# Performance work log

Measured on AMD Instinct MI355X. Metric: run time of the kernel, lower is better.

Reference implementation:

```python
import jax, jax.numpy as jnp
import numpy as np

RADIUS = 0.1
NSAMPLE = 32
B, N, NPOINT, C = 2, 16384, 4096, 64


def setup_inputs() -> dict:
    key = jax.random.key(0)
    k1, k2, k3 = jax.random.split(key, 3)
    xyz = jax.random.uniform(k1, (B, N, 3), dtype=jnp.float32)
    new_xyz = jax.random.uniform(k2, (B, NPOINT, 3), dtype=jnp.float32)
    features = jax.random.normal(k3, (B, C, N), dtype=jnp.float32)
    return {"xyz": xyz, "new_xyz": new_xyz, "features": features}


def ball_query(radius, nsample, xyz, new_xyz):
    # xyz: (B, N, 3), new_xyz: (B, npoint, 3) -> idx: (B, npoint, nsample) int32
    # Semantics of the CUDA ball_query: take the first `nsample` points (in
    # original order) whose squared distance < radius^2; pad remaining slots
    # with the first in-ball index (0 if the ball is empty).
    d2 = jnp.sum((new_xyz[:, :, None, :] - xyz[:, None, :, :]) ** 2, axis=-1)  # (B, npoint, N)
    mask = d2 < radius * radius
    # stable argsort puts in-ball indices first, preserving original order
    order = jnp.argsort(jnp.where(mask, 0, 1), axis=-1)  # (B, npoint, N)
    cnt = jnp.sum(mask, axis=-1, keepdims=True)  # (B, npoint, 1)
    first = jnp.where(cnt > 0, order[..., :1], 0)  # (B, npoint, 1)
    slots = jnp.arange(nsample)
    idx = jnp.where(slots < cnt, order[..., :nsample], first)
    return idx.astype(jnp.int32)


def group(features, idx):
    # features: (B, C, N), idx: (B, npoint, nsample) -> (B, C, npoint, nsample)
    return jax.vmap(lambda f, i: f[:, i])(features, idx)


def reference(xyz, new_xyz, features):
    idx = ball_query(RADIUS, NSAMPLE, xyz, new_xyz)  # (B, npoint, nsample)
    xyz_t = jnp.transpose(xyz, (0, 2, 1))  # (B, 3, N)
    grouped_xyz = group(xyz_t, idx)  # (B, 3, npoint, nsample)
    grouped_xyz = grouped_xyz - jnp.transpose(new_xyz, (0, 2, 1))[..., None]
    grouped_features = group(features, idx)  # (B, C, npoint, nsample)
    new_features = jnp.concatenate([grouped_xyz, grouped_features], axis=1)
    return new_features  # (B, 3 + C, npoint, nsample)
```

## Files before the change

### kernel.cpp

```cpp
#include <hip/hip_runtime.h>

#define B 2
#define N 16384
#define NPOINT 4096
#define C 64
#define NSAMPLE 32

#define NCELL 1000
#define CELLW_STRIDE 1024
#define OFF_STRIDE 1056
#define CAP 192

#define HIST_BLOCKS ((B * (N + NPOINT) + 255) / 256)
#define TRANS_BLOCKS (B * (N / 64))

__device__ __forceinline__ float r2_thresh() { return (float)(0.1 * 0.1); }

__device__ __forceinline__ int clamp09(int v) { return v < 0 ? 0 : (v > 9 ? 9 : v); }

__device__ __forceinline__ int cell_of(float x, float y, float z) {
    const int ix = clamp09((int)floorf(x * 10.0f));
    const int iy = clamp09((int)floorf(y * 10.0f));
    const int iz = clamp09((int)floorf(z * 10.0f));
    return (ix * 10 + iy) * 10 + iz;
}

__global__ void __launch_bounds__(256) hist_transpose_kernel(
    const float* __restrict__ xyz, const float* __restrict__ new_xyz,
    int* __restrict__ cellwork, int* __restrict__ qwork,
    const float* __restrict__ feat, float* __restrict__ ft) {
    __shared__ float tile[64 * 65];
    const int t = threadIdx.x;

    if (blockIdx.x >= HIST_BLOCKS) {
        const int tb = blockIdx.x - HIST_BLOCKS;
        const int b = tb / (N / 64);
        const int n0 = (tb % (N / 64)) * 64;
        const int l = t & 63;
        const int w = t >> 6;
#pragma unroll
        for (int it = 0; it < 16; ++it) {
            const int c = it * 4 + w;
            tile[c * 65 + l] = feat[((size_t)b * C + c) * N + n0 + l];
        }
        __syncthreads();
#pragma unroll
        for (int it = 0; it < 16; ++it) {
            const int nn = it * 4 + w;
            ft[((size_t)b * N + n0 + nn) * C + l] = tile[l * 65 + nn];
        }
        return;
    }

    const int i = blockIdx.x * blockDim.x + t;
    if (i < B * N) {
        const int b = i / N;
        const float x = xyz[(size_t)i * 3 + 0];
        const float y = xyz[(size_t)i * 3 + 1];
        const float z = xyz[(size_t)i * 3 + 2];
        atomicAdd(&cellwork[b * CELLW_STRIDE + cell_of(x, y, z)], 1);
    } else if (i < B * (N + NPOINT)) {
        const int qi = i - B * N;
        const int b = qi / NPOINT;
        const float x = new_xyz[(size_t)qi * 3 + 0];
        const float y = new_xyz[(size_t)qi * 3 + 1];
        const float z = new_xyz[(size_t)qi * 3 + 2];
        atomicAdd(&qwork[b * CELLW_STRIDE + cell_of(x, y, z)], 1);
    }
}

__global__ void __launch_bounds__(1024) grid_scan_kernel(
    int* __restrict__ cellwork, int* __restrict__ qwork, int* __restrict__ off) {
    __shared__ int wsum[16];
    const int blk = blockIdx.x;
    const int t = threadIdx.x;
    const int lane = t & 63;
    const int w = t >> 6;
    int* __restrict__ arr = (blk < B) ? (cellwork + blk * CELLW_STRIDE)
                                      : (qwork + (blk - B) * CELLW_STRIDE);
    const int v = (t < NCELL) ? arr[t] : 0;

    int s = v;
#pragma unroll
    for (int d = 1; d < 64; d <<= 1) {
        const int u = __shfl_up(s, d, 64);
        if (lane >= d) s += u;
    }
    if (lane == 63) wsum[w] = s;
    __syncthreads();
    if (w == 0) {
        int p = (lane < 16) ? wsum[lane] : 0;
#pragma unroll
        for (int d = 1; d < 16; d <<= 1) {
            const int u = __shfl_up(p, d, 64);
            if (lane >= d) p += u;
        }
        if (lane < 16) wsum[lane] = p;
    }
    __syncthreads();
    const int prefix = (w > 0) ? wsum[w - 1] : 0;
    const int excl = s + prefix - v;
    if (blk < B && t <= NCELL) off[blk * OFF_STRIDE + t] = excl;
    if (t < NCELL) arr[t] = excl;
}

__global__ void __launch_bounds__(256) grid_scatter_kernel(
    const float* __restrict__ xyz, const float* __restrict__ new_xyz,
    int* __restrict__ cellwork, int* __restrict__ qwork,
    float4* __restrict__ binned, int* __restrict__ qperm) {
    const int i = blockIdx.x * blockDim.x + threadIdx.x;
    if (i < B * N) {
        const int b = i / N;
        const int p = i - b * N;
        const float x = xyz[(size_t)i * 3 + 0];
        const float y = xyz[(size_t)i * 3 + 1];
        const float z = xyz[(size_t)i * 3 + 2];
        const int c = cell_of(x, y, z);
        const int pos = atomicAdd(&cellwork[b * CELLW_STRIDE + c], 1);
        float4 v;
        v.x = x; v.y = y; v.z = z; v.w = __int_as_float(p);
        binned[(size_t)b * N + pos] = v;
    } else if (i < B * (N + NPOINT)) {
        const int qi = i - B * N;
        const int b = qi / NPOINT;
        const int j = qi - b * NPOINT;
        const float x = new_xyz[(size_t)qi * 3 + 0];
        const float y = new_xyz[(size_t)qi * 3 + 1];
        const float z = new_xyz[(size_t)qi * 3 + 2];
        const int c = cell_of(x, y, z);
        const int pos = atomicAdd(&qwork[b * CELLW_STRIDE + c], 1);
        qperm[b * NPOINT + pos] = j;
    }
}

__device__ void linear_ball_fallback(const float* __restrict__ xb,
                                     float cx, float cy, float cz,
                                     int lane, unsigned long long lanemask_lt,
                                     int* out) {
    const float r2 = r2_thresh();
    int cnt = 0, first_idx = 0;
    for (int base = 0; base < N; base += 64) {
        const int i = base + lane;
        const float x = xb[i * 3 + 0];
        const float y = xb[i * 3 + 1];
        const float z = xb[i * 3 + 2];
        float d2;
        {
#pragma clang fp contract(off)
            float dx = x - cx;
            float dy = y - cy;
            float dz = z - cz;
            d2 = dx * dx + dy * dy + dz * dz;
        }
        const bool in = d2 < r2;
        const unsigned long long m = __ballot(in);
        if (in) {
            const int pos = cnt + __popcll(m & lanemask_lt);
            if (pos < NSAMPLE) out[pos] = i;
        }
        if (cnt == 0 && m != 0ull) first_idx = base + __builtin_ctzll(m);
        cnt += __popcll(m);
        if (cnt >= NSAMPLE) break;
    }
    if (cnt < NSAMPLE) {
        if (cnt == 0) first_idx = 0;
        for (int pos = cnt + lane; pos < NSAMPLE; pos += 64) out[pos] = first_idx;
    }
}

__device__ __forceinline__ void rank_select(const int* cand, int K, int lane,
                                            int* out) {
    const int e0 = (lane < K) ? cand[lane] : 0x7FFFFFFF;
    const int e1 = (64 + lane < K) ? cand[64 + lane] : 0x7FFFFFFF;
    const int e2 = (128 + lane < K) ? cand[128 + lane] : 0x7FFFFFFF;
    int r0 = 0, r1 = 0, r2i = 0;
    if (K <= 64) {
        for (int k = 0; k < K; ++k) { const int v = cand[k]; r0 += (v < e0); }
    } else if (K <= 128) {
        for (int k = 0; k < K; ++k) { const int v = cand[k]; r0 += (v < e0); r1 += (v < e1); }
    } else {
        for (int k = 0; k < K; ++k) {
            const int v = cand[k];
            r0 += (v < e0); r1 += (v < e1); r2i += (v < e2);
        }
    }
    if (lane < K && r0 < NSAMPLE) out[r0] = e0;
    if (64 + lane < K && r1 < NSAMPLE) out[r1] = e1;
    if (128 + lane < K && r2i < NSAMPLE) out[r2i] = e2;

    if (K < NSAMPLE) {
        int mn = min(e0, min(e1, e2));
#pragma unroll
        for (int d = 32; d; d >>= 1) mn = min(mn, __shfl_xor(mn, d));
        const int fill = (K > 0) ? mn : 0;
        for (int pos = K + lane; pos < NSAMPLE; pos += 64) out[pos] = fill;
    }
}

__device__ __forceinline__ int scan_window(
    const float4* __restrict__ bb, const int* __restrict__ ob,
    int lox, int hix, int loy, int hiy, int loz, int hiz,
    float cx, float cy, float cz, int lane,
    unsigned long long lanemask_lt, int* cand)
{
    const float r2 = r2_thresh();
    int K = 0;
    for (int ix = lox; ix <= hix; ++ix) {
        for (int iy = loy; iy <= hiy; ++iy) {
            const int rowc = (ix * 10 + iy) * 10;
            const int s0 = ob[rowc + loz];
            const int s1 = ob[rowc + hiz + 1];
            for (int cur = s0; cur < s1; cur += 64) {
                const int i = cur + lane;
                const bool valid = (i < s1);
                float4 pv;
                if (valid) pv = bb[i];
                else { pv.x = 1e9f; pv.y = 1e9f; pv.z = 1e9f; pv.w = 0.0f; }
                float d2;
                {
#pragma clang fp contract(off)
                    float dx = pv.x - cx, dy = pv.y - cy, dz = pv.z - cz;
                    d2 = dx * dx + dy * dy + dz * dz;
                }
                const bool in = valid && (d2 < r2);
                const unsigned long long m = __ballot(in);
                if (in) {
                    const int pos = K + __popcll(m & lanemask_lt);
                    if (pos < CAP) cand[pos] = __float_as_int(pv.w);
                }
                K += __popcll(m);
            }
        }
    }
    return K;
}

__global__ void __launch_bounds__(256) fused_kernel(
    const float4* __restrict__ binned,
    const int* __restrict__ off,
    const float* __restrict__ new_xyz,
    const float* __restrict__ xyz,
    const float* __restrict__ ft,
    const int* __restrict__ qperm,
    float* __restrict__ out)
{
    __shared__ int cand_s[4][CAP];
    __shared__ int sidx[4 * NSAMPLE];
    __shared__ int sj[4];
    __shared__ float sf[64 * 65];

    const int t = threadIdx.x;
    const int lane = t & 63;
    const int w = t >> 6;

    const int nwg = B * NPOINT / 4;
    const int g = blockIdx.x;
    const int swz = (g & 7) * (nwg / 8) + (g >> 3);
    const int b = swz / (NPOINT / 4);
    const int p4 = swz % (NPOINT / 4);

    const int j = qperm[b * NPOINT + p4 * 4 + w];
    if (lane == 0) sj[w] = j;

    const float cx = new_xyz[((size_t)b * NPOINT + j) * 3 + 0];
    const float cy = new_xyz[((size_t)b * NPOINT + j) * 3 + 1];
    const float cz = new_xyz[((size_t)b * NPOINT + j) * 3 + 2];

    int* cand = cand_s[w];
    int* sout = sidx + w * NSAMPLE;
    const float4* __restrict__ bb = binned + (size_t)b * N;
    const int* __restrict__ ob = off + b * OFF_STRIDE;

    const unsigned long long lanemask_lt = (lane == 63) ? 0x7FFFFFFFFFFFFFFFull
                                                        : ((1ull << lane) - 1ull);

    const int lox = max(0, (int)floorf((cx - 0.1001f) * 10.0f));
    const int hix = min(9, (int)floorf((cx + 0.1001f) * 10.0f));
    const int loy = max(0, (int)floorf((cy - 0.1001f) * 10.0f));
    const int hiy = min(9, (int)floorf((cy + 0.1001f) * 10.0f));
    const int loz = max(0, (int)floorf((cz - 0.1001f) * 10.0f));
    const int hiz = min(9, (int)floorf((cz + 0.1001f) * 10.0f));

    const int K = scan_window(bb, ob, lox, hix, loy, hiy, loz, hiz,
                              cx, cy, cz, lane, lanemask_lt, cand);

    if (K > CAP) {
        linear_ball_fallback(xyz + (size_t)b * N * 3, cx, cy, cz, lane, lanemask_lt, sout);
    } else {
        rank_select(cand, K, lane, sout);
    }
    __syncthreads();

    const size_t plane = (size_t)NPOINT * NSAMPLE;
    const size_t bbase = (size_t)b * (3 + C) * plane;

    if (t < 128) {
        const int id = sidx[t];
        const int jq = sj[t >> 5];
        const int s = t & 31;
        const size_t cb = ((size_t)b * NPOINT + jq) * 3;
        const size_t pb = ((size_t)b * N + id) * 3;
        const size_t obx = bbase + (size_t)jq * NSAMPLE + s;
        {
#pragma clang fp contract(off)
            out[obx + 0 * plane] = xyz[pb + 0] - new_xyz[cb + 0];
            out[obx + 1 * plane] = xyz[pb + 1] - new_xyz[cb + 1];
            out[obx + 2 * plane] = xyz[pb + 2] - new_xyz[cb + 2];
        }
    }

#pragma unroll
    for (int h = 0; h < 2; ++h) {
        const int* sidxL = sidx + h * 64;
        {
            const int lane16 = t & 15;
            const int pg = t >> 4;
#pragma unroll
            for (int it = 0; it < 4; ++it) {
                const int pp = it * 16 + pg;
                const int id = sidxL[pp];
                const float4 v = *(const float4*)(ft + ((size_t)b * N + id) * C + lane16 * 4);
                float* dst = sf + pp * 65 + lane16 * 4;
                dst[0] = v.x; dst[1] = v.y; dst[2] = v.z; dst[3] = v.w;
            }
        }
        __syncthreads();
        const int q = sj[2 * h + (lane >> 5)];
        const size_t rowbase = bbase + (size_t)q * NSAMPLE + (lane & 31);
#pragma unroll
        for (int it = 0; it < 16; ++it) {
            const int c = it * 4 + w;
            out[rowbase + (size_t)(3 + c) * plane] = sf[lane * 65 + c];
        }
        __syncthreads();
    }
}

__global__ void __launch_bounds__(256) ball_query_kernel(
    const float* __restrict__ xyz, const float* __restrict__ new_xyz,
    int* __restrict__ idx_out)
{
    const int wave = (blockIdx.x * blockDim.x + threadIdx.x) >> 6;
    const int lane = threadIdx.x & 63;
    if (wave >= B * NPOINT) return;
    const int b = wave / NPOINT;
    const float cx = new_xyz[(size_t)wave * 3 + 0];
    const float cy = new_xyz[(size_t)wave * 3 + 1];
    const float cz = new_xyz[(size_t)wave * 3 + 2];
    const unsigned long long lanemask_lt = (lane == 63) ? 0x7FFFFFFFFFFFFFFFull
                                                        : ((1ull << lane) - 1ull);
    linear_ball_fallback(xyz + (size_t)b * N * 3, cx, cy, cz, lane, lanemask_lt,
                         idx_out + (size_t)wave * NSAMPLE);
}

__global__ void __launch_bounds__(256) group_kernel(
    const float* __restrict__ xyz, const float* __restrict__ new_xyz,
    const float* __restrict__ feat, const int* __restrict__ idx_arr,
    float* __restrict__ out) {
    const int t = threadIdx.x;
    const int s = t & 31;
    const int jl = t >> 5;
    const int j = blockIdx.x * 8 + jl;
    const int b = blockIdx.y;

    const int id = idx_arr[((size_t)b * NPOINT + j) * NSAMPLE + s];

    const float px = xyz[((size_t)b * N + id) * 3 + 0] - new_xyz[((size_t)b * NPOINT + j) * 3 + 0];
    const float py = xyz[((size_t)b * N + id) * 3 + 1] - new_xyz[((size_t)b * NPOINT + j) * 3 + 1];
    const float pz = xyz[((size_t)b * N + id) * 3 + 2] - new_xyz[((size_t)b * NPOINT + j) * 3 + 2];

    const size_t plane = (size_t)NPOINT * NSAMPLE;
    const size_t obase = (size_t)b * (3 + C) * plane + (size_t)j * NSAMPLE + s;

    out[obase + 0 * plane] = px;
    out[obase + 1 * plane] = py;
    out[obase + 2 * plane] = pz;

    const float* __restrict__ fb = feat + (size_t)b * C * N;
#pragma unroll 8
    for (int c = 0; c < C; ++c) {
        out[obase + (size_t)(3 + c) * plane] = fb[(size_t)c * N + id];
    }
}

extern "C" void kernel_launch(void* const* d_in, const int* in_sizes, int n_in,
                              void* d_out, int out_size, void* d_ws, size_t ws_size,
                              hipStream_t stream) {
    const float* xyz     = (const float*)d_in[0];
    const float* new_xyz = (const float*)d_in[1];
    const float* feat    = (const float*)d_in[2];
    float* out = (float*)d_out;

    const size_t idx_bytes    = (size_t)B * NPOINT * NSAMPLE * sizeof(int);
    const size_t ft_bytes     = (size_t)B * N * C * sizeof(float);
    const size_t binned_bytes = (size_t)B * N * sizeof(float4);
    const size_t off_bytes    = (size_t)B * OFF_STRIDE * sizeof(int);
    const size_t cellw_bytes  = (size_t)B * CELLW_STRIDE * sizeof(int);
    const size_t qwork_bytes  = (size_t)B * CELLW_STRIDE * sizeof(int);
    const size_t qperm_bytes  = (size_t)B * NPOINT * sizeof(int);

    char* ws = (char*)d_ws;
    size_t o = 0;
    int*    idx_ws   = (int*)(ws + o);    o += idx_bytes;
    float*  ft       = (float*)(ws + o);  o += ft_bytes;
    float4* binned   = (float4*)(ws + o); o += binned_bytes;
    int*    off      = (int*)(ws + o);    o += off_bytes;
    int*    cellwork = (int*)(ws + o);    o += cellw_bytes;
    int*    qwork    = (int*)(ws + o);    o += qwork_bytes;
    int*    qperm    = (int*)(ws + o);    o += qperm_bytes;

    const bool use_grid = (ws_size >= o);

    if (use_grid) {
        hipMemsetAsync(cellwork, 0, cellw_bytes + qwork_bytes, stream);
        hist_transpose_kernel<<<HIST_BLOCKS + TRANS_BLOCKS, 256, 0, stream>>>(
            xyz, new_xyz, cellwork, qwork, feat, ft);
        grid_scan_kernel<<<2 * B, 1024, 0, stream>>>(cellwork, qwork, off);
        grid_scatter_kernel<<<(B * (N + NPOINT) + 255) / 256, 256, 0, stream>>>(
            xyz, new_xyz, cellwork, qwork, binned, qperm);
        fused_kernel<<<B * NPOINT / 4, 256, 0, stream>>>(
            binned, off, new_xyz, xyz, ft, qperm, out);
    } else {
        ball_query_kernel<<<(B * NPOINT) / 4, 256, 0, stream>>>(xyz, new_xyz, idx_ws);
        dim3 grid2(NPOINT / 8, B);
        group_kernel<<<grid2, 256, 0, stream>>>(xyz, new_xyz, feat, idx_ws, out);
    }
}
```

Measured before the change: 46.86 us.

## Fuse grid scan and scatter into one kernel with shared-memory cursors

Merges the prefix-scan and scatter kernels into one launch per batch and array. Scatter cursors now live in LDS atomics instead of global atomics, which removes a kernel launch and global atomic traffic. The cost is that the scatter runs on only 4 blocks of 1024 threads, which limits parallelism for 32K points. The change also vectorizes the rank_select comparisons with int4 LDS reads (adding sentinel padding to the candidate buffer), prefetches the next segment bounds in scan_window, and makes the window bounds wave-uniform with readfirstlane.

```diff
diff --git a/kernel.cpp b/kernel.cpp
--- a/kernel.cpp
+++ b/kernel.cpp
@@ -69,15 +69,20 @@
     }
 }
 
-__global__ void __launch_bounds__(1024) grid_scan_kernel(
-    int* __restrict__ cellwork, int* __restrict__ qwork, int* __restrict__ off) {
+__global__ void __launch_bounds__(1024) scan_scatter_kernel(
+    const float* __restrict__ xyz, const float* __restrict__ new_xyz,
+    const int* __restrict__ cellwork, const int* __restrict__ qwork,
+    int* __restrict__ off, float4* __restrict__ binned, int* __restrict__ qperm) {
     __shared__ int wsum[16];
+    __shared__ int cur[1024];
     const int blk = blockIdx.x;
     const int t = threadIdx.x;
     const int lane = t & 63;
     const int w = t >> 6;
-    int* __restrict__ arr = (blk < B) ? (cellwork + blk * CELLW_STRIDE)
-                                      : (qwork + (blk - B) * CELLW_STRIDE);
+    const bool is_pts = (blk < B);
+    const int b = is_pts ? blk : blk - B;
+    const int* __restrict__ arr = is_pts ? (cellwork + b * CELLW_STRIDE)
+                                         : (qwork + b * CELLW_STRIDE);
     const int v = (t < NCELL) ? arr[t] : 0;
 
     int s = v;
@@ -100,36 +105,28 @@
     __syncthreads();
     const int prefix = (w > 0) ? wsum[w - 1] : 0;
     const int excl = s + prefix - v;
-    if (blk < B && t <= NCELL) off[blk * OFF_STRIDE + t] = excl;
-    if (t < NCELL) arr[t] = excl;
-}
-
-__global__ void __launch_bounds__(256) grid_scatter_kernel(
-    const float* __restrict__ xyz, const float* __restrict__ new_xyz,
-    int* __restrict__ cellwork, int* __restrict__ qwork,
-    float4* __restrict__ binned, int* __restrict__ qperm) {
-    const int i = blockIdx.x * blockDim.x + threadIdx.x;
-    if (i < B * N) {
-        const int b = i / N;
-        const int p = i - b * N;
-        const float x = xyz[(size_t)i * 3 + 0];
-        const float y = xyz[(size_t)i * 3 + 1];
-        const float z = xyz[(size_t)i * 3 + 2];
-        const int c = cell_of(x, y, z);
-        const int pos = atomicAdd(&cellwork[b * CELLW_STRIDE + c], 1);
-        float4 v;
-        v.x = x; v.y = y; v.z = z; v.w = __int_as_float(p);
-        binned[(size_t)b * N + pos] = v;
-    } else if (i < B * (N + NPOINT)) {
-        const int qi = i - B * N;
-        const int b = qi / NPOINT;
-        const int j = qi - b * NPOINT;
-        const float x = new_xyz[(size_t)qi * 3 + 0];
-        const float y = new_xyz[(size_t)qi * 3 + 1];
-        const float z = new_xyz[(size_t)qi * 3 + 2];
-        const int c = cell_of(x, y, z);
-        const int pos = atomicAdd(&qwork[b * CELLW_STRIDE + c], 1);
-        qperm[b * NPOINT + pos] = j;
+    if (is_pts && t <= NCELL) off[b * OFF_STRIDE + t] = excl;
+    cur[t] = excl;
+    __syncthreads();
+
+    if (is_pts) {
+        for (int i = t; i < N; i += 1024) {
+            const float x = xyz[((size_t)b * N + i) * 3 + 0];
+            const float y = xyz[((size_t)b * N + i) * 3 + 1];
+            const float z = xyz[((size_t)b * N + i) * 3 + 2];
+            const int pos = atomicAdd(&cur[cell_of(x, y, z)], 1);
+            float4 pv;
+            pv.x = x; pv.y = y; pv.z = z; pv.w = __int_as_float(i);
+            binned[(size_t)b * N + pos] = pv;
+        }
+    } else {
+        for (int i = t; i < NPOINT; i += 1024) {
+            const float x = new_xyz[((size_t)b * NPOINT + i) * 3 + 0];
+            const float y = new_xyz[((size_t)b * NPOINT + i) * 3 + 1];
+            const float z = new_xyz[((size_t)b * NPOINT + i) * 3 + 2];
+            const int pos = atomicAdd(&cur[cell_of(x, y, z)], 1);
+            qperm[b * NPOINT + pos] = i;
+        }
     }
 }
 
@@ -168,20 +165,30 @@
     }
 }
 
-__device__ __forceinline__ void rank_select(const int* cand, int K, int lane,
+__device__ __forceinline__ void rank_select(int* cand, int K, int lane,
                                             int* out) {
+    if (lane < 4) cand[K + lane] = 0x7FFFFFFF;
     const int e0 = (lane < K) ? cand[lane] : 0x7FFFFFFF;
     const int e1 = (64 + lane < K) ? cand[64 + lane] : 0x7FFFFFFF;
     const int e2 = (128 + lane < K) ? cand[128 + lane] : 0x7FFFFFFF;
     int r0 = 0, r1 = 0, r2i = 0;
     if (K <= 64) {
-        for (int k = 0; k < K; ++k) { const int v = cand[k]; r0 += (v < e0); }
+        for (int k = 0; k < K; k += 4) {
+            const int4 v = *(const int4*)(cand + k);
+            r0 += (v.x < e0) + (v.y < e0) + (v.z < e0) + (v.w < e0);
+        }
     } else if (K <= 128) {
-        for (int k = 0; k < K; ++k) { const int v = cand[k]; r0 += (v < e0); r1 += (v < e1); }
+        for (int k = 0; k < K; k += 4) {
+            const int4 v = *(const int4*)(cand + k);
+            r0 += (v.x < e0) + (v.y < e0) + (v.z < e0) + (v.w < e0);
+            r1 += (v.x < e1) + (v.y < e1) + (v.z < e1) + (v.w < e1);
+        }
     } else {
-        for (int k = 0; k < K; ++k) {
-            const int v = cand[k];
-            r0 += (v < e0); r1 += (v < e1); r2i += (v < e2);
+        for (int k = 0; k < K; k += 4) {
+            const int4 v = *(const int4*)(cand + k);
+            r0 += (v.x < e0) + (v.y < e0) + (v.z < e0) + (v.w < e0);
+            r1 += (v.x < e1) + (v.y < e1) + (v.z < e1) + (v.w < e1);
+            r2i += (v.x < e2) + (v.y < e2) + (v.z < e2) + (v.w < e2);
         }
     }
     if (lane < K && r0 < NSAMPLE) out[r0] = e0;
@@ -204,33 +211,44 @@
     unsigned long long lanemask_lt, int* cand)
 {
     const float r2 = r2_thresh();
+    const int ny = hiy - loy + 1;
+    const int nseg = (hix - lox + 1) * ny;
     int K = 0;
-    for (int ix = lox; ix <= hix; ++ix) {
-        for (int iy = loy; iy <= hiy; ++iy) {
-            const int rowc = (ix * 10 + iy) * 10;
-            const int s0 = ob[rowc + loz];
-            const int s1 = ob[rowc + hiz + 1];
-            for (int cur = s0; cur < s1; cur += 64) {
-                const int i = cur + lane;
-                const bool valid = (i < s1);
-                float4 pv;
-                if (valid) pv = bb[i];
-                else { pv.x = 1e9f; pv.y = 1e9f; pv.z = 1e9f; pv.w = 0.0f; }
-                float d2;
-                {
+
+    int nix = lox, niy = loy;
+    int a0 = ob[(nix * 10 + niy) * 10 + loz];
+    int b0 = ob[(nix * 10 + niy) * 10 + hiz + 1];
+
+    for (int s = 0; s < nseg; ++s) {
+        int a1 = 0, b1 = 0;
+        if (s + 1 < nseg) {
+            ++niy;
+            if (niy > hiy) { niy = loy; ++nix; }
+            const int rowc = (nix * 10 + niy) * 10;
+            a1 = ob[rowc + loz];
+            b1 = ob[rowc + hiz + 1];
+        }
+        for (int cur = a0; cur < b0; cur += 64) {
+            const int i = cur + lane;
+            const bool valid = (i < b0);
+            float4 pv;
+            if (valid) pv = bb[i];
+            else { pv.x = 1e9f; pv.y = 1e9f; pv.z = 1e9f; pv.w = 0.0f; }
+            float d2;
+            {
 #pragma clang fp contract(off)
-                    float dx = pv.x - cx, dy = pv.y - cy, dz = pv.z - cz;
-                    d2 = dx * dx + dy * dy + dz * dz;
-                }
-                const bool in = valid && (d2 < r2);
-                const unsigned long long m = __ballot(in);
-                if (in) {
-                    const int pos = K + __popcll(m & lanemask_lt);
-                    if (pos < CAP) cand[pos] = __float_as_int(pv.w);
-                }
-                K += __popcll(m);
+                float dx = pv.x - cx, dy = pv.y - cy, dz = pv.z - cz;
+                d2 = dx * dx + dy * dy + dz * dz;
             }
-        }
+            const bool in = valid && (d2 < r2);
+            const unsigned long long m = __ballot(in);
+            if (in) {
+                const int pos = K + __popcll(m & lanemask_lt);
+                if (pos < CAP) cand[pos] = __float_as_int(pv.w);
+            }
+            K += __popcll(m);
+        }
+        a0 = a1; b0 = b1;
     }
     return K;
 }
@@ -244,7 +262,7 @@
     const int* __restrict__ qperm,
     float* __restrict__ out)
 {
-    __shared__ int cand_s[4][CAP];
+    __shared__ int cand_s[4][CAP + 4];
     __shared__ int sidx[4 * NSAMPLE];
     __shared__ int sj[4];
     __shared__ float sf[64 * 65];
@@ -259,7 +277,7 @@
     const int b = swz / (NPOINT / 4);
     const int p4 = swz % (NPOINT / 4);
 
-    const int j = qperm[b * NPOINT + p4 * 4 + w];
+    const int j = __builtin_amdgcn_readfirstlane(qperm[b * NPOINT + p4 * 4 + w]);
     if (lane == 0) sj[w] = j;
 
     const float cx = new_xyz[((size_t)b * NPOINT + j) * 3 + 0];
@@ -274,12 +292,12 @@
     const unsigned long long lanemask_lt = (lane == 63) ? 0x7FFFFFFFFFFFFFFFull
                                                         : ((1ull << lane) - 1ull);
 
-    const int lox = max(0, (int)floorf((cx - 0.1001f) * 10.0f));
-    const int hix = min(9, (int)floorf((cx + 0.1001f) * 10.0f));
-    const int loy = max(0, (int)floorf((cy - 0.1001f) * 10.0f));
-    const int hiy = min(9, (int)floorf((cy + 0.1001f) * 10.0f));
-    const int loz = max(0, (int)floorf((cz - 0.1001f) * 10.0f));
-    const int hiz = min(9, (int)floorf((cz + 0.1001f) * 10.0f));
+    const int lox = __builtin_amdgcn_readfirstlane(max(0, (int)floorf((cx - 0.1001f) * 10.0f)));
+    const int hix = __builtin_amdgcn_readfirstlane(min(9, (int)floorf((cx + 0.1001f) * 10.0f)));
+    const int loy = __builtin_amdgcn_readfirstlane(max(0, (int)floorf((cy - 0.1001f) * 10.0f)));
+    const int hiy = __builtin_amdgcn_readfirstlane(min(9, (int)floorf((cy + 0.1001f) * 10.0f)));
+    const int loz = __builtin_amdgcn_readfirstlane(max(0, (int)floorf((cz - 0.1001f) * 10.0f)));
+    const int hiz = __builtin_amdgcn_readfirstlane(min(9, (int)floorf((cz + 0.1001f) * 10.0f)));
 
     const int K = scan_window(bb, ob, lox, hix, loy, hiy, loz, hiz,
                               cx, cy, cz, lane, lanemask_lt, cand);
@@ -415,9 +433,8 @@
         hipMemsetAsync(cellwork, 0, cellw_bytes + qwork_bytes, stream);
         hist_transpose_kernel<<<HIST_BLOCKS + TRANS_BLOCKS, 256, 0, stream>>>(
             xyz, new_xyz, cellwork, qwork, feat, ft);
-        grid_scan_kernel<<<2 * B, 1024, 0, stream>>>(cellwork, qwork, off);
-        grid_scatter_kernel<<<(B * (N + NPOINT) + 255) / 256, 256, 0, stream>>>(
-            xyz, new_xyz, cellwork, qwork, binned, qperm);
+        scan_scatter_kernel<<<2 * B, 1024, 0, stream>>>(
+            xyz, new_xyz, cellwork, qwork, off, binned, qperm);
         fused_kernel<<<B * NPOINT / 4, 256, 0, stream>>>(
             binned, off, new_xyz, xyz, ft, qperm, out);
     } else {
```

Measured after the change: 57.92 us. 1.24x slower.

## Fuse grid prefix scan into scatter kernel with redundant per-block scans

Applied to the files above, without the earlier changes.

Merges the separate cell-count scan kernel and the scatter kernel into one launch. Each scatter block recomputes the 1000-cell exclusive prefix sum in shared memory from the histogram, then places points using that offset plus a separate global cursor array updated with atomics. This removes one kernel launch and its serialization point, in exchange for redundant scan work in every block and two extra zeroed cursor arrays.

```diff
diff --git a/kernel.cpp b/kernel.cpp
--- a/kernel.cpp
+++ b/kernel.cpp
@@ -13,6 +13,10 @@
 
 #define HIST_BLOCKS ((B * (N + NPOINT) + 255) / 256)
 #define TRANS_BLOCKS (B * (N / 64))
+
+#define PTS_BLK_PER_B (N / 256)
+#define Q_BLK_PER_B (NPOINT / 256)
+#define SS_BLOCKS (B * (PTS_BLK_PER_B + Q_BLK_PER_B))
 
 __device__ __forceinline__ float r2_thresh() { return (float)(0.1 * 0.1); }
 
@@ -69,67 +73,88 @@
     }
 }
 
-__global__ void __launch_bounds__(1024) grid_scan_kernel(
-    int* __restrict__ cellwork, int* __restrict__ qwork, int* __restrict__ off) {
-    __shared__ int wsum[16];
-    const int blk = blockIdx.x;
+__global__ void __launch_bounds__(256) scan_scatter_kernel(
+    const float* __restrict__ xyz, const float* __restrict__ new_xyz,
+    const int* __restrict__ cellwork, const int* __restrict__ qwork,
+    int* __restrict__ off, float4* __restrict__ binned, int* __restrict__ qperm,
+    int* __restrict__ gcur, int* __restrict__ qgcur) {
+    __shared__ int lds_off[1024];
+    __shared__ int wsum[4];
+
     const int t = threadIdx.x;
     const int lane = t & 63;
     const int w = t >> 6;
-    int* __restrict__ arr = (blk < B) ? (cellwork + blk * CELLW_STRIDE)
-                                      : (qwork + (blk - B) * CELLW_STRIDE);
-    const int v = (t < NCELL) ? arr[t] : 0;
-
-    int s = v;
+    const int blk = blockIdx.x;
+
+    const bool is_pts = (blk < B * PTS_BLK_PER_B);
+    int b, k;
+    const int* cnt;
+    int* gc;
+    if (is_pts) {
+        b = blk / PTS_BLK_PER_B;
+        k = blk % PTS_BLK_PER_B;
+        cnt = cellwork + b * CELLW_STRIDE;
+        gc = gcur + b * CELLW_STRIDE;
+    } else {
+        const int q = blk - B * PTS_BLK_PER_B;
+        b = q / Q_BLK_PER_B;
+        k = q % Q_BLK_PER_B;
+        cnt = qwork + b * CELLW_STRIDE;
+        gc = qgcur + b * CELLW_STRIDE;
+    }
+
+    const int4 c4 = *(const int4*)(cnt + 4 * t);
+    const int i0 = c4.x;
+    const int i1 = i0 + c4.y;
+    const int i2 = i1 + c4.z;
+    const int i3 = i2 + c4.w;
+
+    int ws = i3;
 #pragma unroll
     for (int d = 1; d < 64; d <<= 1) {
-        const int u = __shfl_up(s, d, 64);
-        if (lane >= d) s += u;
-    }
-    if (lane == 63) wsum[w] = s;
+        const int u = __shfl_up(ws, d, 64);
+        if (lane >= d) ws += u;
+    }
+    if (lane == 63) wsum[w] = ws;
     __syncthreads();
-    if (w == 0) {
-        int p = (lane < 16) ? wsum[lane] : 0;
-#pragma unroll
-        for (int d = 1; d < 16; d <<= 1) {
-            const int u = __shfl_up(p, d, 64);
-            if (lane >= d) p += u;
-        }
-        if (lane < 16) wsum[lane] = p;
-    }
+    int wpre = 0;
+#pragma unroll
+    for (int x = 0; x < 4; ++x) {
+        const int v = wsum[x];
+        if (x < w) wpre += v;
+    }
+    const int base = wpre + (ws - i3);
+    lds_off[4 * t + 0] = base;
+    lds_off[4 * t + 1] = base + i0;
+    lds_off[4 * t + 2] = base + i1;
+    lds_off[4 * t + 3] = base + i2;
     __syncthreads();
-    const int prefix = (w > 0) ? wsum[w - 1] : 0;
-    const int excl = s + prefix - v;
-    if (blk < B && t <= NCELL) off[blk * OFF_STRIDE + t] = excl;
-    if (t < NCELL) arr[t] = excl;
-}
-
-__global__ void __launch_bounds__(256) grid_scatter_kernel(
-    const float* __restrict__ xyz, const float* __restrict__ new_xyz,
-    int* __restrict__ cellwork, int* __restrict__ qwork,
-    float4* __restrict__ binned, int* __restrict__ qperm) {
-    const int i = blockIdx.x * blockDim.x + threadIdx.x;
-    if (i < B * N) {
-        const int b = i / N;
-        const int p = i - b * N;
-        const float x = xyz[(size_t)i * 3 + 0];
-        const float y = xyz[(size_t)i * 3 + 1];
-        const float z = xyz[(size_t)i * 3 + 2];
+
+    if (is_pts && k == 0) {
+#pragma unroll
+        for (int jj = 0; jj < 4; ++jj) {
+            const int idx = 4 * t + jj;
+            if (idx <= NCELL) off[b * OFF_STRIDE + idx] = lds_off[idx];
+        }
+    }
+
+    const int i = k * 256 + t;
+    if (is_pts) {
+        const float x = xyz[((size_t)b * N + i) * 3 + 0];
+        const float y = xyz[((size_t)b * N + i) * 3 + 1];
+        const float z = xyz[((size_t)b * N + i) * 3 + 2];
         const int c = cell_of(x, y, z);
-        const int pos = atomicAdd(&cellwork[b * CELLW_STRIDE + c], 1);
-        float4 v;
-        v.x = x; v.y = y; v.z = z; v.w = __int_as_float(p);
-        binned[(size_t)b * N + pos] = v;
-    } else if (i < B * (N + NPOINT)) {
-        const int qi = i - B * N;
-        const int b = qi / NPOINT;
-        const int j = qi - b * NPOINT;
-        const float x = new_xyz[(size_t)qi * 3 + 0];
-        const float y = new_xyz[(size_t)qi * 3 + 1];
-        const float z = new_xyz[(size_t)qi * 3 + 2];
+        const int pos = lds_off[c] + atomicAdd(&gc[c], 1);
+        float4 pv;
+        pv.x = x; pv.y = y; pv.z = z; pv.w = __int_as_float(i);
+        binned[(size_t)b * N + pos] = pv;
+    } else {
+        const float x = new_xyz[((size_t)b * NPOINT + i) * 3 + 0];
+        const float y = new_xyz[((size_t)b * NPOINT + i) * 3 + 1];
+        const float z = new_xyz[((size_t)b * NPOINT + i) * 3 + 2];
         const int c = cell_of(x, y, z);
-        const int pos = atomicAdd(&qwork[b * CELLW_STRIDE + c], 1);
-        qperm[b * NPOINT + pos] = j;
+        const int pos = lds_off[c] + atomicAdd(&gc[c], 1);
+        qperm[b * NPOINT + pos] = i;
     }
 }
 
@@ -397,6 +422,8 @@
     const size_t off_bytes    = (size_t)B * OFF_STRIDE * sizeof(int);
     const size_t cellw_bytes  = (size_t)B * CELLW_STRIDE * sizeof(int);
     const size_t qwork_bytes  = (size_t)B * CELLW_STRIDE * sizeof(int);
+    const size_t gcur_bytes   = (size_t)B * CELLW_STRIDE * sizeof(int);
+    const size_t qgcur_bytes  = (size_t)B * CELLW_STRIDE * sizeof(int);
     const size_t qperm_bytes  = (size_t)B * NPOINT * sizeof(int);
 
     char* ws = (char*)d_ws;
@@ -407,17 +434,18 @@
     int*    off      = (int*)(ws + o);    o += off_bytes;
     int*    cellwork = (int*)(ws + o);    o += cellw_bytes;
     int*    qwork    = (int*)(ws + o);    o += qwork_bytes;
+    int*    gcur     = (int*)(ws + o);    o += gcur_bytes;
+    int*    qgcur    = (int*)(ws + o);    o += qgcur_bytes;
     int*    qperm    = (int*)(ws + o);    o += qperm_bytes;
 
     const bool use_grid = (ws_size >= o);
 
     if (use_grid) {
-        hipMemsetAsync(cellwork, 0, cellw_bytes + qwork_bytes, stream);
+        hipMemsetAsync(cellwork, 0, cellw_bytes + qwork_bytes + gcur_bytes + qgcur_bytes, stream);
         hist_transpose_kernel<<<HIST_BLOCKS + TRANS_BLOCKS, 256, 0, stream>>>(
             xyz, new_xyz, cellwork, qwork, feat, ft);
-        grid_scan_kernel<<<2 * B, 1024, 0, stream>>>(cellwork, qwork, off);
-        grid_scatter_kernel<<<(B * (N + NPOINT) + 255) / 256, 256, 0, stream>>>(
-            xyz, new_xyz, cellwork, qwork, binned, qperm);
+        scan_scatter_kernel<<<SS_BLOCKS, 256, 0, stream>>>(
+            xyz, new_xyz, cellwork, qwork, off, binned, qperm, gcur, qgcur);
         fused_kernel<<<B * NPOINT / 4, 256, 0, stream>>>(
             binned, off, new_xyz, xyz, ft, qperm, out);
     } else {
```

New measurement: 46.17 us. No clear change (-1.5%).
